# Kernel optimization log

Hardware: AMD Instinct MI355X
Metric: run time of the kernel (lower is better)

The kernel has to match this reference:

```python
import jax, jax.numpy as jnp
import numpy as np
import math

D_MODEL = 512
NHEAD = 8
NUM_LAYERS = 3
FF_HIDDEN = 512
B, LQ, LK = 4, 1024, 2048
LN_EPS = 1e-5


def _mha(q_in, k_in, v_in, Wq, Wk, Wv, Wo, nhead, mask):
    # Weights stored [d_in, d_out]; torch Linear(bias=False) is x @ W.T, we fold the
    # transpose into storage so math is identical.
    Bq, Lq, d = q_in.shape
    dh = d // nhead
    # NOTE: original uses .view(B, nhead, -1, dh) on contiguous [B, L, d] — a plain
    # row-major reshape, NOT the usual transpose head split. Replicate exactly.
    q = (q_in @ Wq).reshape(Bq, nhead, -1, dh)
    k = (k_in @ Wk).reshape(Bq, nhead, -1, dh)
    v = (v_in @ Wv).reshape(Bq, nhead, -1, dh)
    u = jnp.einsum('bhqd,bhkd->bhqk', q, k) / math.sqrt(dh)
    if mask is not None:
        m = mask[:, None]  # broadcast over heads
        u = jnp.where(m, -jnp.inf, u)
    attn = jax.nn.softmax(u, axis=-1)
    if mask is not None:
        attn = jnp.where(m, 0.0, attn)
    out = jnp.einsum('bhqk,bhkd->bhqd', attn, v).reshape(Bq, Lq, d)
    return out @ Wo


def _layernorm(x, g, b):
    mu = jnp.mean(x, axis=-1, keepdims=True)
    var = jnp.mean((x - mu) ** 2, axis=-1, keepdims=True)
    return (x - mu) * jax.lax.rsqrt(var + LN_EPS) * g + b


def setup_inputs() -> dict:
    key = jax.random.key(0)
    ks = jax.random.split(key, 16)
    d, L, f = D_MODEL, NUM_LAYERS, FF_HIDDEN
    s = 0.02
    inp = {
        'x': jax.random.normal(ks[0], (B, LK, d), jnp.float32),
        'h': jax.random.normal(ks[1], (B, LQ, d), jnp.float32),
        'mask': jax.random.randint(ks[2], (B, LQ, LK), 0, 10) == 0,
        'wq': jax.random.normal(ks[3], (L, d, d), jnp.float32) * s,
        'wk': jax.random.normal(ks[4], (L, d, d), jnp.float32) * s,
        'wv': jax.random.normal(ks[5], (L, d, d), jnp.float32) * s,
        'wo': jax.random.normal(ks[6], (L, d, d), jnp.float32) * s,
        'ffw1': jax.random.normal(ks[7], (L, d, f), jnp.float32) * s,
        'ffb1': jnp.zeros((L, f), jnp.float32),
        'ffw2': jax.random.normal(ks[8], (L, f, d), jnp.float32) * s,
        'ffb2': jnp.zeros((L, d), jnp.float32),
        'g1': jnp.ones((L, d), jnp.float32),
        'be1': jnp.zeros((L, d), jnp.float32),
        'g2': jnp.ones((L, d), jnp.float32),
        'be2': jnp.zeros((L, d), jnp.float32),
        'out_wq': jax.random.normal(ks[9], (d, d), jnp.float32) * s,
        'out_wk': jax.random.normal(ks[10], (d, d), jnp.float32) * s,
    }
    return inp


def reference(x, h, mask, wq, wk, wv, wo, ffw1, ffb1, ffw2, ffb2, g1, be1, g2, be2, out_wq, out_wk):
    L = wq.shape[0]
    for i in range(L):
        a = _mha(h, x, x, wq[i], wk[i], wv[i], wo[i], NHEAD, mask)
        h = _layernorm(h + a, g1[i], be1[i])
        ff = jax.nn.relu(h @ ffw1[i] + ffb1[i]) @ ffw2[i] + ffb2[i]
        h = _layernorm(h + ff, g2[i], be2[i])
    # output MHA with nhead=1, output_attention=True: returns u.mean(dim=1)
    d = h.shape[-1]
    q = (h @ out_wq)[:, None]  # [B,1,Lq,d]
    k = (x @ out_wk)[:, None]  # [B,1,Lk,d]
    u = jnp.einsum('bhqd,bhkd->bhqk', q, k) / math.sqrt(d)
    # mean over head dim of size 1; torch .squeeze(1) is a no-op since Lq > 1
    return u.mean(axis=1)  # [B, Lq, Lk]
```

## Files before the change

### kernel.cpp

```cpp
#include <hip/hip_runtime.h>
#include <math.h>


#define D_MODEL 512
#define LQ 1024
#define LKK 2048
#define BB 4
#define NL 3
#define KSPLIT 2
#define NROWS 32768
#define WSZC 262144L

typedef __bf16 bf16;
typedef __bf16 bf16x8 __attribute__((ext_vector_type(8)));
typedef __bf16 bf16x4 __attribute__((ext_vector_type(4)));
typedef float f32x4 __attribute__((ext_vector_type(4)));

__device__ inline f32x4 mfma16(bf16x8 a, bf16x8 b, f32x4 c) {
    return __builtin_amdgcn_mfma_f32_16x16x32_bf16(a, b, c, 0, 0, 0);
}

__device__ inline void gload16(const void* g, void* l) {
    __builtin_amdgcn_global_load_lds(
        (const __attribute__((address_space(1))) void*)g,
        (__attribute__((address_space(3))) void*)l, 16, 0, 0);
}

__device__ inline float fexp2(float x) { return __builtin_amdgcn_exp2f(x); }

__global__ __launch_bounds__(256) void cast_kernel(
    const float* __restrict__ in, bf16* __restrict__ out, long n)
{
    long i4 = ((long)blockIdx.x * 256 + threadIdx.x) * 4;
    if (i4 >= n) return;
    float4 v = *(const float4*)(in + i4);
    bf16x4 o;
    o[0] = (bf16)v.x; o[1] = (bf16)v.y; o[2] = (bf16)v.z; o[3] = (bf16)v.w;
    *(bf16x4*)(out + i4) = o;
}

__global__ __launch_bounds__(256) void tcast_all(
    const float* __restrict__ wq, const float* __restrict__ wo,
    const float* __restrict__ f1, const float* __restrict__ f2,
    const float* __restrict__ wk, const float* __restrict__ wv,
    const float* __restrict__ owq, const float* __restrict__ owk,
    bf16* __restrict__ wts, bf16* __restrict__ wtOQ)
{
    __shared__ float t[32][33];
    int z = blockIdx.z;
    const float* src; bf16* dst;
    if (z < 3)       { src = wq  + z * WSZC;        dst = wts + (long)z * WSZC; }
    else if (z < 6)  { src = wo  + (z - 3) * WSZC;  dst = wts + (long)z * WSZC; }
    else if (z < 9)  { src = f1  + (z - 6) * WSZC;  dst = wts + (long)z * WSZC; }
    else if (z < 12) { src = f2  + (z - 9) * WSZC;  dst = wts + (long)z * WSZC; }
    else if (z < 15) { src = wk  + (z - 12) * WSZC; dst = wts + (12 + 2 * (z - 12)) * WSZC; }
    else if (z < 18) { src = wv  + (z - 15) * WSZC; dst = wts + (13 + 2 * (z - 15)) * WSZC; }
    else if (z == 18){ src = owq;                   dst = wtOQ; }
    else             { src = owk;                   dst = wts + 18 * WSZC; }

    int tx = threadIdx.x & 31, ty = threadIdx.x >> 5;
    int x0 = blockIdx.x * 32, y0 = blockIdx.y * 32;
#pragma unroll
    for (int i = 0; i < 4; i++)
        t[ty + 8 * i][tx] = src[(long)(y0 + ty + 8 * i) * 512 + x0 + tx];
    __syncthreads();
#pragma unroll
    for (int i = 0; i < 4; i++)
        dst[(long)(x0 + ty + 8 * i) * 512 + y0 + tx] = (bf16)t[tx][ty + 8 * i];
}

__global__ __launch_bounds__(256) void maskbits_kernel(
    const int* __restrict__ m, unsigned* __restrict__ bits)
{
    long i = (long)blockIdx.x * 256 + threadIdx.x;
    int v = m[i] != 0;
    unsigned long long bal = __ballot(v);
    int lane = threadIdx.x & 63;
    if (lane == 0) bits[i >> 5] = (unsigned)bal;
    else if (lane == 32) bits[i >> 5] = (unsigned)(bal >> 32);
}

__global__ __launch_bounds__(256) void vtrans_kernel(
    const bf16* __restrict__ v, bf16* __restrict__ vt)
{
    __shared__ bf16 t[64][72];
    int bh = blockIdx.y;
    int p0 = blockIdx.x * 64;
    const bf16* vb = v + ((long)bh * 2048 + p0) * 64;
    bf16* vtb = vt + (long)bh * 64 * 2048;
    int tid = threadIdx.x;
#pragma unroll
    for (int it = 0; it < 2; it++) {
        int r = it * 32 + (tid >> 3);
        int c8 = (tid & 7) * 8;
        bf16x8 vv = *(const bf16x8*)(vb + (long)r * 64 + c8);
        *(bf16x8*)&t[r][c8] = vv;
    }
    __syncthreads();
#pragma unroll
    for (int it = 0; it < 2; it++) {
        int d = it * 32 + (tid >> 3);
        int p8 = (tid & 7) * 8;
        bf16x8 ov;
#pragma unroll
        for (int j = 0; j < 8; j++) ov[j] = t[p8 + j][d];
        *(bf16x8*)(vtb + (long)d * 2048 + p0 + p8) = ov;
    }
}

template<int BIAS, int RELU, int OUT_BF16>
__global__ __launch_bounds__(256) void mfma_gemm(
    const bf16* __restrict__ A, const bf16* __restrict__ Bt,
    const float* __restrict__ bias, void* __restrict__ Cv,
    int N, int K)
{
    __shared__ bf16 As[2][4096];
    __shared__ bf16 Bs[2][2048];
    int tid = threadIdx.x;
    int lane = tid & 63, w = tid >> 6;
    int wr = w >> 1, wc = w & 1;
    int g = lane >> 4, c = lane & 15;
    long row0 = (long)blockIdx.y * 128;
    int n0 = blockIdx.x * 64;

    f32x4 acc[4][2];
#pragma unroll
    for (int m = 0; m < 4; m++)
#pragma unroll
        for (int n = 0; n < 2; n++) acc[m][n] = (f32x4){0.f, 0.f, 0.f, 0.f};

    int lr4 = lane >> 2, lc8 = (lane & 3) * 8;
    auto STAGE = [&](int buf, int k0) {
        const bf16* ga = A + (row0 + w * 32 + lr4) * (long)K + k0 + lc8;
        gload16(ga, &As[buf][(w * 32) * 32]);
        gload16(ga + (long)16 * K, &As[buf][(w * 32 + 16) * 32]);
        const bf16* gb = Bt + (long)(n0 + w * 16 + lr4) * K + k0 + lc8;
        gload16(gb, &Bs[buf][(w * 16) * 32]);
    };

    STAGE(0, 0);
    __syncthreads();
    int nk = K >> 5;
    for (int it = 0; it < nk; ++it) {
        int cur = it & 1;
        if (it + 1 < nk) STAGE(cur ^ 1, (it + 1) << 5);
        bf16x8 af[4], bfr[2];
#pragma unroll
        for (int m = 0; m < 4; m++)
            af[m] = *(const bf16x8*)&As[cur][(wr * 64 + m * 16 + c) * 32 + g * 8];
#pragma unroll
        for (int n = 0; n < 2; n++)
            bfr[n] = *(const bf16x8*)&Bs[cur][(wc * 32 + n * 16 + c) * 32 + g * 8];
#pragma unroll
        for (int m = 0; m < 4; m++)
#pragma unroll
            for (int n = 0; n < 2; n++)
                acc[m][n] = mfma16(af[m], bfr[n], acc[m][n]);
        __syncthreads();
    }

    float bv[2] = {0.f, 0.f};
    if (BIAS) {
#pragma unroll
        for (int n = 0; n < 2; n++) bv[n] = bias[n0 + wc * 32 + n * 16 + c];
    }
    float* Cf = (float*)Cv;
    bf16* Cb = (bf16*)Cv;
#pragma unroll
    for (int m = 0; m < 4; m++)
#pragma unroll
        for (int n = 0; n < 2; n++)
#pragma unroll
            for (int j = 0; j < 4; j++) {
                long row = row0 + wr * 64 + m * 16 + g * 4 + j;
                int col = n0 + wc * 32 + n * 16 + c;
                float v = acc[m][n][j];
                if (BIAS) v += bv[n];
                if (RELU) v = fmaxf(v, 0.f);
                if (OUT_BF16) Cb[row * N + col] = (bf16)v;
                else Cf[row * N + col] = v;
            }
}

template<int OUT_BF16>
__device__ inline void gemm128_body(
    const bf16* __restrict__ Ab, const bf16* __restrict__ Bb,
    void* __restrict__ Cv, int N, int K, float scale,
    long row0, int n0)
{
    __shared__ bf16 As[2][4096];
    __shared__ bf16 Bs[2][4096];
    int tid = threadIdx.x;
    int lane = tid & 63, w = tid >> 6;
    int wr = w >> 1, wc = w & 1;
    int g = lane >> 4, c = lane & 15;

    f32x4 acc[4][4];
#pragma unroll
    for (int m = 0; m < 4; m++)
#pragma unroll
        for (int n = 0; n < 4; n++) acc[m][n] = (f32x4){0.f, 0.f, 0.f, 0.f};

    int lr4 = lane >> 2, lc8 = (lane & 3) * 8;
    auto STAGE = [&](int buf, int k0) {
        const bf16* ga = Ab + (row0 + w * 16 + lr4) * (long)K + k0 + lc8;
        gload16(ga, &As[buf][(w * 16) * 32]);
        gload16(ga + (long)64 * K, &As[buf][(w * 16 + 64) * 32]);
        const bf16* gb = Bb + (long)(n0 + w * 16 + lr4) * K + k0 + lc8;
        gload16(gb, &Bs[buf][(w * 16) * 32]);
        gload16(gb + (long)64 * K, &Bs[buf][(w * 16 + 64) * 32]);
    };

    STAGE(0, 0);
    __syncthreads();
    int nk = K >> 5;
    for (int it = 0; it < nk; ++it) {
        int cur = it & 1;
        if (it + 1 < nk) STAGE(cur ^ 1, (it + 1) << 5);
        bf16x8 af[4], bfr[4];
#pragma unroll
        for (int m = 0; m < 4; m++)
            af[m] = *(const bf16x8*)&As[cur][(wr * 64 + m * 16 + c) * 32 + g * 8];
#pragma unroll
        for (int n = 0; n < 4; n++)
            bfr[n] = *(const bf16x8*)&Bs[cur][(wc * 64 + n * 16 + c) * 32 + g * 8];
#pragma unroll
        for (int m = 0; m < 4; m++)
#pragma unroll
            for (int n = 0; n < 4; n++)
                acc[m][n] = mfma16(af[m], bfr[n], acc[m][n]);
        __syncthreads();
    }

    float* Cf = (float*)Cv;
    bf16* Cb = (bf16*)Cv;
#pragma unroll
    for (int m = 0; m < 4; m++)
#pragma unroll
        for (int n = 0; n < 4; n++)
#pragma unroll
            for (int j = 0; j < 4; j++) {
                long row = row0 + wr * 64 + m * 16 + g * 4 + j;
                int col = n0 + wc * 64 + n * 16 + c;
                float v = acc[m][n][j] * scale;
                if (OUT_BF16) Cb[row * N + col] = (bf16)v;
                else Cf[row * N + col] = v;
            }
}

__global__ __launch_bounds__(256) void mfma_gemm128(
    const bf16* __restrict__ A, const bf16* __restrict__ Bt,
    float* __restrict__ Cv, int N, int K, float scale,
    long sA, long sB, long sC)
{
    long z = blockIdx.z;
    gemm128_body<0>(A + z * sA, Bt + z * sB, Cv + z * sC, N, K, scale,
                    (long)blockIdx.y * 128, blockIdx.x * 128);
}

__global__ __launch_bounds__(256) void qkv_gemm(
    const bf16* __restrict__ Ah, const bf16* __restrict__ Ax,
    const bf16* __restrict__ B0, const bf16* __restrict__ B1,
    const bf16* __restrict__ B2,
    bf16* __restrict__ C0, bf16* __restrict__ C1, bf16* __restrict__ C2,
    float scale0)
{
    int z = blockIdx.z;
    if (z == 0 && blockIdx.y >= 32) return;
    const bf16* A = z ? Ax : Ah;
    const bf16* Bt = (z == 0) ? B0 : (z == 1 ? B1 : B2);
    bf16* C = (z == 0) ? C0 : (z == 1 ? C1 : C2);
    gemm128_body<1>(A, Bt, C, 512, 512, z == 0 ? scale0 : 1.f,
                    (long)blockIdx.y * 128, blockIdx.x * 128);
}

__global__ __launch_bounds__(256, 4) void attn_mfma(
    const bf16* __restrict__ QP, const bf16* __restrict__ KP,
    const bf16* __restrict__ Vt, const unsigned* __restrict__ bits,
    bf16* __restrict__ Opart, float* __restrict__ Mpart,
    float* __restrict__ Lpart)
{
    __shared__ bf16 Kls[2][4096];
    __shared__ bf16 Vls[2][4096];
    __shared__ bf16 Pl[4][1024];

    int tid = threadIdx.x;
    int lane = tid & 63, wv = tid >> 6;
    int g = lane >> 4, c = lane & 15;

    int flat = blockIdx.x;
    int logical = (flat & 7) * 128 + (flat >> 3);
    int bh = logical >> 5;
    int rr = logical & 31;
    int sp = rr >> 4;
    int q0 = (rr & 15) * 64 + wv * 16;
    int b = bh >> 3;

    long qrow0 = (long)bh * 1024 + q0;
    long krow0 = (long)bh * 2048 + (long)sp * 1024;
    const bf16* vtb = Vt + (long)bh * 131072 + (long)sp * 1024;
    const unsigned* bitrow = bits + ((long)b * 1024 + q0 + c) * 64 + sp * 32;

    int lr = lane >> 3, lc = lane & 7;
    int scol = (lc ^ lr) * 8;
    int cs = c & 7;

    bf16x8 qa[2];
#pragma unroll
    for (int hh = 0; hh < 2; hh++)
        qa[hh] = *(const bf16x8*)(QP + (qrow0 + c) * 64 + hh * 32 + g * 8);

    f32x4 o_acc[4];
#pragma unroll
    for (int ot = 0; ot < 4; ot++) o_acc[ot] = (f32x4){0.f, 0.f, 0.f, 0.f};
    float m_r = -1e30f, l_r = 0.f;

    {
        const bf16* sk = KP + (krow0 + wv * 16 + lr) * 64 + scol;
        gload16(sk, &Kls[0][(wv * 16) * 64]);
        gload16(sk + 8 * 64, &Kls[0][(wv * 16 + 8) * 64]);
        const bf16* sv = vtb + (long)(wv * 16 + lr) * 2048 + scol;
        gload16(sv, &Vls[0][(wv * 16) * 64]);
        gload16(sv + 8 * 2048, &Vls[0][(wv * 16 + 8) * 64]);
    }
    uint2 wp_nxt = *(const uint2*)(bitrow);
    __syncthreads();

    const int NT = LKK / KSPLIT / 64;
    for (int kt = 0; kt < NT; kt++) {
        int cur = kt & 1;
        if (kt + 1 < NT) {
            int kn = (kt + 1) * 64;
            const bf16* sk = KP + (krow0 + kn + wv * 16 + lr) * 64 + scol;
            gload16(sk, &Kls[cur ^ 1][(wv * 16) * 64]);
            gload16(sk + 8 * 64, &Kls[cur ^ 1][(wv * 16 + 8) * 64]);
            const bf16* sv = vtb + (long)(wv * 16 + lr) * 2048 + kn + scol;
            gload16(sv, &Vls[cur ^ 1][(wv * 16) * 64]);
            gload16(sv + 8 * 2048, &Vls[cur ^ 1][(wv * 16 + 8) * 64]);
        }
        uint2 wp = wp_nxt;
        if (kt + 1 < NT) wp_nxt = *(const uint2*)(bitrow + (kt + 1) * 2);

        const char* kls = (const char*)&Kls[cur][0];
        f32x4 s[4];
#pragma unroll
        for (int mt = 0; mt < 4; mt++) {
            bf16x8 ka0 = *(const bf16x8*)(kls + (mt * 16 + c) * 128 + ((g ^ cs) << 4));
            bf16x8 ka1 = *(const bf16x8*)(kls + (mt * 16 + c) * 128 + (((4 + g) ^ cs) << 4));
            s[mt] = mfma16(ka0, qa[0], (f32x4){0.f, 0.f, 0.f, 0.f});
            s[mt] = mfma16(ka1, qa[1], s[mt]);
        }

#pragma unroll
        for (int mt = 0; mt < 4; mt++)
#pragma unroll
            for (int j = 0; j < 4; j++) {
                int kl = mt * 16 + 4 * g + j;
                unsigned wsel = (kl < 32) ? wp.x : wp.y;
                if ((wsel >> (kl & 31)) & 1) s[mt][j] = -1e30f;
            }

        float mx = -1e30f;
#pragma unroll
        for (int mt = 0; mt < 4; mt++)
            mx = fmaxf(mx, fmaxf(fmaxf(s[mt][0], s[mt][1]),
                                 fmaxf(s[mt][2], s[mt][3])));
        mx = fmaxf(mx, __shfl_xor(mx, 16, 64));
        mx = fmaxf(mx, __shfl_xor(mx, 32, 64));

        float fct = 1.f;
        if (__any(mx > m_r + 11.5415f)) {
            float mnew = fmaxf(m_r, mx);
            fct = fexp2(m_r - mnew);
            m_r = mnew;
            float fq[4];
#pragma unroll
            for (int j = 0; j < 4; j++)
                fq[j] = __shfl(fct, (lane & 48) | (4 * g + j), 64);
#pragma unroll
            for (int ot = 0; ot < 4; ot++)
#pragma unroll
                for (int j = 0; j < 4; j++) o_acc[ot][j] *= fq[j];
        }

        float sum = 0.f;
#pragma unroll
        for (int mt = 0; mt < 4; mt++)
#pragma unroll
            for (int j = 0; j < 4; j++) {
                float p = fexp2(s[mt][j] - m_r);
                s[mt][j] = p;
                sum += p;
            }
        sum += __shfl_xor(sum, 16, 64);
        sum += __shfl_xor(sum, 32, 64);
        l_r = l_r * fct + sum;

        char* plb = (char*)&Pl[wv][0];
#pragma unroll
        for (int mt = 0; mt < 4; mt++) {
            bf16x4 pk;
#pragma unroll
            for (int j = 0; j < 4; j++) pk[j] = (bf16)s[mt][j];
            int wch = (mt * 2 + (g >> 1)) ^ cs;
            *(bf16x4*)(plb + c * 128 + (wch << 4) + (g & 1) * 8) = pk;
        }

        const char* vls = (const char*)&Vls[cur][0];
#pragma unroll
        for (int kh = 0; kh < 2; kh++) {
            bf16x8 pa = *(const bf16x8*)(plb + c * 128 + ((((kh << 2) + g) ^ cs) << 4));
#pragma unroll
            for (int ot = 0; ot < 4; ot++) {
                bf16x8 vbf = *(const bf16x8*)
                    (vls + (ot * 16 + c) * 128 + ((((kh << 2) + g) ^ cs) << 4));
                o_acc[ot] = mfma16(pa, vbf, o_acc[ot]);
            }
        }
        __syncthreads();
    }

    long ob = ((long)sp * NROWS + qrow0) * 64;
#pragma unroll
    for (int ot = 0; ot < 4; ot++)
#pragma unroll
        for (int j = 0; j < 4; j++)
            Opart[ob + (long)(4 * g + j) * 64 + ot * 16 + c] = (bf16)o_acc[ot][j];
    if (g == 0) {
        Mpart[(long)sp * NROWS + qrow0 + c] = m_r;
        Lpart[(long)sp * NROWS + qrow0 + c] = l_r;
    }
}

__global__ __launch_bounds__(256) void attn_combine(
    const bf16* __restrict__ Op, const float* __restrict__ Mp,
    const float* __restrict__ Lp, bf16* __restrict__ O)
{
    long idx = (long)blockIdx.x * 256 + threadIdx.x;
    long row = idx >> 6;
    float m0 = Mp[row], m1 = Mp[NROWS + row];
    float l0 = Lp[row], l1 = Lp[NROWS + row];
    float mm = fmaxf(m0, m1);
    float e0 = fexp2(m0 - mm), e1 = fexp2(m1 - mm);
    float inv = 1.f / (l0 * e0 + l1 * e1);
    float o = ((float)Op[idx] * e0 + (float)Op[(long)NROWS * 64 + idx] * e1) * inv;
    O[idx] = (bf16)o;
}

__global__ __launch_bounds__(256) void ln_kernel(
    const float* __restrict__ res, const float* __restrict__ y,
    const float* __restrict__ g, const float* __restrict__ bb,
    float* __restrict__ outf, bf16* __restrict__ outb)
{
    int wave = threadIdx.x >> 6, lane = threadIdx.x & 63;
    long row = (long)blockIdx.x * 4 + wave;
    const float* rp = res + row * D_MODEL;
    const float* yp = y + row * D_MODEL;
    float v[8];
    float s = 0.f, sq = 0.f;
#pragma unroll
    for (int j = 0; j < 8; j++) {
        int col = lane + 64 * j;
        v[j] = rp[col] + yp[col];
        s += v[j]; sq += v[j] * v[j];
    }
#pragma unroll
    for (int o = 32; o > 0; o >>= 1) {
        s += __shfl_down(s, o, 64);
        sq += __shfl_down(sq, o, 64);
    }
    s = __shfl(s, 0, 64);
    sq = __shfl(sq, 0, 64);
    float mean = s * (1.f / 512.f);
    float var = sq * (1.f / 512.f) - mean * mean;
    float rstd = rsqrtf(fmaxf(var, 0.f) + 1e-5f);
    float* opf = outf + row * D_MODEL;
    bf16* opb = outb + row * D_MODEL;
#pragma unroll
    for (int j = 0; j < 8; j++) {
        int col = lane + 64 * j;
        float o = (v[j] - mean) * rstd * g[col] + bb[col];
        opf[col] = o;
        opb[col] = (bf16)o;
    }
}

extern "C" void kernel_launch(void* const* d_in, const int* in_sizes, int n_in,
                              void* d_out, int out_size, void* d_ws, size_t ws_size,
                              hipStream_t stream)
{
    const float* x    = (const float*)d_in[0];
    const float* hin  = (const float*)d_in[1];
    const int*   mask = (const int*)d_in[2];
    const float* wq   = (const float*)d_in[3];
    const float* wk   = (const float*)d_in[4];
    const float* wv   = (const float*)d_in[5];
    const float* wo   = (const float*)d_in[6];
    const float* ffw1 = (const float*)d_in[7];
    const float* ffb1 = (const float*)d_in[8];
    const float* ffw2 = (const float*)d_in[9];
    const float* ffb2 = (const float*)d_in[10];
    const float* g1   = (const float*)d_in[11];
    const float* be1  = (const float*)d_in[12];
    const float* g2   = (const float*)d_in[13];
    const float* be2  = (const float*)d_in[14];
    const float* out_wq = (const float*)d_in[15];
    const float* out_wk = (const float*)d_in[16];
    float* out = (float*)d_out;

    const long NQ = (long)BB * LQ;
    const long NK = (long)BB * LKK;

    char* W = (char*)d_ws;
    float* h_f  = (float*)(W);
    char*  SH   = W + 8388608;
    float* y_f  = (float*)SH;
    bf16*  v_pl = (bf16*)SH;
    bf16*  opart= (bf16*)SH;
    bf16*  h_b  = (bf16*)(W + 16777216);
    bf16*  x_b  = (bf16*)(W + 20971520);
    bf16*  q_b  = (bf16*)(W + 29360128);
    bf16*  a_b  = (bf16*)(W + 33554432);
    bf16*  k_pl = (bf16*)(W + 37748736);
    bf16*  vt   = (bf16*)(W + 46137344);
    bf16*  wts  = (bf16*)(W + 54525952);
    bf16*  wtOQ = wts + 19 * WSZC;
    unsigned* mb = (unsigned*)(W + 65011712);
    float* Mpart = (float*)(W + 66060288);
    float* Lpart = (float*)(W + 66322432);

    dim3 blk(256);

    hipMemcpyAsync(h_f, hin, NQ * D_MODEL * sizeof(float),
                   hipMemcpyDeviceToDevice, stream);
    cast_kernel<<<dim3((NK * D_MODEL / 4 + 255) / 256), blk, 0, stream>>>(x, x_b, NK * D_MODEL);
    cast_kernel<<<dim3((NQ * D_MODEL / 4 + 255) / 256), blk, 0, stream>>>(hin, h_b, NQ * D_MODEL);
    tcast_all<<<dim3(16, 16, 20), blk, 0, stream>>>(
        wq, wo, ffw1, ffw2, wk, wv, out_wq, out_wk, wts, wtOQ);
    maskbits_kernel<<<dim3(32768), blk, 0, stream>>>(mask, mb);

    dim3 gq(8, 32, 1);
    dim3 gqkv(4, 64, 3);
    dim3 gvt(32, 32);
    dim3 ga(1024);
    dim3 gc(NROWS * 64 / 256);

    const float C2 = 0.1803368801111243f;

    for (int i = 0; i < NL; i++) {
        qkv_gemm<<<gqkv, blk, 0, stream>>>(h_b, x_b,
            wts + i * WSZC, wts + (12 + 2 * i) * WSZC, wts + (13 + 2 * i) * WSZC,
            q_b, k_pl, v_pl, C2);
        vtrans_kernel<<<gvt, blk, 0, stream>>>(v_pl, vt);

        attn_mfma<<<ga, blk, 0, stream>>>(q_b, k_pl, vt, mb, opart, Mpart, Lpart);
        attn_combine<<<gc, blk, 0, stream>>>(opart, Mpart, Lpart, a_b);

        mfma_gemm<0,0,0><<<gq, blk, 0, stream>>>(a_b, wts + (3 + i) * WSZC,
            nullptr, y_f, 512, 512);
        ln_kernel<<<dim3(NQ / 4), blk, 0, stream>>>(h_f, y_f,
            g1 + i * D_MODEL, be1 + i * D_MODEL, h_f, h_b);

        mfma_gemm<1,1,1><<<gq, blk, 0, stream>>>(h_b, wts + (6 + i) * WSZC,
            ffb1 + i * D_MODEL, q_b, 512, 512);
        mfma_gemm<1,0,0><<<gq, blk, 0, stream>>>(q_b, wts + (9 + i) * WSZC,
            ffb2 + i * D_MODEL, y_f, 512, 512);
        ln_kernel<<<dim3(NQ / 4), blk, 0, stream>>>(h_f, y_f,
            g2 + i * D_MODEL, be2 + i * D_MODEL, h_f, h_b);
    }

    dim3 gqk(4, 64, 2);
    qkv_gemm<<<gqk, blk, 0, stream>>>(h_b, x_b,
        wtOQ, wts + 18 * WSZC, wts + 18 * WSZC, q_b, k_pl, k_pl, 1.f);

    dim3 gf(LKK / 128, LQ / 128, BB);
    mfma_gemm128<<<gf, blk, 0, stream>>>(q_b, k_pl, out,
        LKK, 512, 0.04419417382415922f,
        (long)LQ * 512, (long)LKK * 512, (long)LQ * LKK);
}
```

Before: 410.7 us.

## Widen GEMM K-tile with swizzled LDS, add MFMA priority hints, fuse h copy into cast

The generic MFMA GEMM now stages 64-wide K slices instead of 32, using an XOR-swizzled LDS layout to avoid bank conflicts. This halves the number of barrier iterations and doubles LDS use per block. The attention kernel wraps its MFMA sections in s_setprio to favour matrix issue over other waves. The device-to-device memcpy of h is folded into a dual-output cast kernel, removing one pass over the input.

Result: no change. 403.6 us (-1.7%).

```diff
diff --git a/kernel.cpp b/kernel.cpp
--- a/kernel.cpp
+++ b/kernel.cpp
@@ -37,6 +37,19 @@
     bf16x4 o;
     o[0] = (bf16)v.x; o[1] = (bf16)v.y; o[2] = (bf16)v.z; o[3] = (bf16)v.w;
     *(bf16x4*)(out + i4) = o;
+}
+
+__global__ __launch_bounds__(256) void cast_dual(
+    const float* __restrict__ in, float* __restrict__ outf,
+    bf16* __restrict__ outb, long n)
+{
+    long i4 = ((long)blockIdx.x * 256 + threadIdx.x) * 4;
+    if (i4 >= n) return;
+    float4 v = *(const float4*)(in + i4);
+    *(float4*)(outf + i4) = v;
+    bf16x4 o;
+    o[0] = (bf16)v.x; o[1] = (bf16)v.y; o[2] = (bf16)v.z; o[3] = (bf16)v.w;
+    *(bf16x4*)(outb + i4) = o;
 }
 
 __global__ __launch_bounds__(256) void tcast_all(
@@ -114,8 +127,8 @@
     const float* __restrict__ bias, void* __restrict__ Cv,
     int N, int K)
 {
-    __shared__ bf16 As[2][4096];
-    __shared__ bf16 Bs[2][2048];
+    __shared__ bf16 As[2][8192];
+    __shared__ bf16 Bs[2][4096];
     int tid = threadIdx.x;
     int lane = tid & 63, w = tid >> 6;
     int wr = w >> 1, wc = w & 1;
@@ -129,33 +142,47 @@
 #pragma unroll
         for (int n = 0; n < 2; n++) acc[m][n] = (f32x4){0.f, 0.f, 0.f, 0.f};
 
-    int lr4 = lane >> 2, lc8 = (lane & 3) * 8;
+    int lr8 = lane >> 3;
+    int scol = ((lane & 7) ^ lr8) * 8;
+    int cs = c & 7;
+
     auto STAGE = [&](int buf, int k0) {
-        const bf16* ga = A + (row0 + w * 32 + lr4) * (long)K + k0 + lc8;
-        gload16(ga, &As[buf][(w * 32) * 32]);
-        gload16(ga + (long)16 * K, &As[buf][(w * 32 + 16) * 32]);
-        const bf16* gb = Bt + (long)(n0 + w * 16 + lr4) * K + k0 + lc8;
-        gload16(gb, &Bs[buf][(w * 16) * 32]);
+#pragma unroll
+        for (int i = 0; i < 4; i++) {
+            const bf16* ga = A + (row0 + w * 32 + i * 8 + lr8) * (long)K + k0 + scol;
+            gload16(ga, &As[buf][(w * 32 + i * 8) * 64]);
+        }
+#pragma unroll
+        for (int j = 0; j < 2; j++) {
+            const bf16* gb = Bt + (long)(n0 + w * 16 + j * 8 + lr8) * K + k0 + scol;
+            gload16(gb, &Bs[buf][(w * 16 + j * 8) * 64]);
+        }
     };
 
     STAGE(0, 0);
     __syncthreads();
-    int nk = K >> 5;
+    int nk = K >> 6;
     for (int it = 0; it < nk; ++it) {
         int cur = it & 1;
-        if (it + 1 < nk) STAGE(cur ^ 1, (it + 1) << 5);
-        bf16x8 af[4], bfr[2];
-#pragma unroll
-        for (int m = 0; m < 4; m++)
-            af[m] = *(const bf16x8*)&As[cur][(wr * 64 + m * 16 + c) * 32 + g * 8];
-#pragma unroll
-        for (int n = 0; n < 2; n++)
-            bfr[n] = *(const bf16x8*)&Bs[cur][(wc * 32 + n * 16 + c) * 32 + g * 8];
-#pragma unroll
-        for (int m = 0; m < 4; m++)
+        if (it + 1 < nk) STAGE(cur ^ 1, (it + 1) << 6);
+#pragma unroll
+        for (int kk = 0; kk < 2; kk++) {
+            int ch = ((kk << 2) + g);
+            bf16x8 af[4], bfr[2];
+#pragma unroll
+            for (int m = 0; m < 4; m++)
+                af[m] = *(const bf16x8*)
+                    &As[cur][(wr * 64 + m * 16 + c) * 64 + ((ch ^ cs) << 3)];
 #pragma unroll
             for (int n = 0; n < 2; n++)
-                acc[m][n] = mfma16(af[m], bfr[n], acc[m][n]);
+                bfr[n] = *(const bf16x8*)
+                    &Bs[cur][(wc * 32 + n * 16 + c) * 64 + ((ch ^ cs) << 3)];
+#pragma unroll
+            for (int m = 0; m < 4; m++)
+#pragma unroll
+                for (int n = 0; n < 2; n++)
+                    acc[m][n] = mfma16(af[m], bfr[n], acc[m][n]);
+        }
         __syncthreads();
     }
 
@@ -343,6 +370,7 @@
 
         const char* kls = (const char*)&Kls[cur][0];
         f32x4 s[4];
+        __builtin_amdgcn_s_setprio(1);
 #pragma unroll
         for (int mt = 0; mt < 4; mt++) {
             bf16x8 ka0 = *(const bf16x8*)(kls + (mt * 16 + c) * 128 + ((g ^ cs) << 4));
@@ -350,6 +378,7 @@
             s[mt] = mfma16(ka0, qa[0], (f32x4){0.f, 0.f, 0.f, 0.f});
             s[mt] = mfma16(ka1, qa[1], s[mt]);
         }
+        __builtin_amdgcn_s_setprio(0);
 
 #pragma unroll
         for (int mt = 0; mt < 4; mt++)
@@ -407,6 +436,7 @@
         }
 
         const char* vls = (const char*)&Vls[cur][0];
+        __builtin_amdgcn_s_setprio(1);
 #pragma unroll
         for (int kh = 0; kh < 2; kh++) {
             bf16x8 pa = *(const bf16x8*)(plb + c * 128 + ((((kh << 2) + g) ^ cs) << 4));
@@ -417,6 +447,7 @@
                 o_acc[ot] = mfma16(pa, vbf, o_acc[ot]);
             }
         }
+        __builtin_amdgcn_s_setprio(0);
         __syncthreads();
     }
 
@@ -531,10 +562,8 @@
 
     dim3 blk(256);
 
-    hipMemcpyAsync(h_f, hin, NQ * D_MODEL * sizeof(float),
-                   hipMemcpyDeviceToDevice, stream);
     cast_kernel<<<dim3((NK * D_MODEL / 4 + 255) / 256), blk, 0, stream>>>(x, x_b, NK * D_MODEL);
-    cast_kernel<<<dim3((NQ * D_MODEL / 4 + 255) / 256), blk, 0, stream>>>(hin, h_b, NQ * D_MODEL);
+    cast_dual<<<dim3((NQ * D_MODEL / 4 + 255) / 256), blk, 0, stream>>>(hin, h_f, h_b, NQ * D_MODEL);
     tcast_all<<<dim3(16, 16, 20), blk, 0, stream>>>(
         wq, wo, ffw1, ffw2, wk, wv, out_wq, out_wk, wts, wtOQ);
     maskbits_kernel<<<dim3(32768), blk, 0, stream>>>(mask, mb);
```
